# Performance work log

Measured on AMD Instinct MI355X. Metric: run time of the kernel, lower is better.

## Reference

```python
import jax, jax.numpy as jnp
import numpy as np

EMBED_DIM = 1024
HEADS = 16
D_HEAD = EMBED_DIM // HEADS
B, S = 4, 2048


def setup_inputs() -> dict:
    key = jax.random.key(0)
    ks = jax.random.split(key, 7)
    scale = 1.0 / np.sqrt(EMBED_DIM)
    inp = {
        "key": jax.random.normal(ks[0], (B, S, EMBED_DIM), jnp.float32),
        "query": jax.random.normal(ks[1], (B, S, EMBED_DIM), jnp.float32),
        "value": jax.random.normal(ks[2], (B, S, EMBED_DIM), jnp.float32),
        # causal boolean mask, broadcastable to [B, H, S, S]
        "mask": jnp.tril(jnp.ones((S, S), dtype=bool))[None, None, :, :] * jnp.ones((B, 1, 1, 1), dtype=bool),
        # nn.Linear weights, stored torch-style as [out_features, in_features]
        "Wq": jax.random.normal(ks[3], (EMBED_DIM, EMBED_DIM), jnp.float32) * scale,
        "Wk": jax.random.normal(ks[4], (EMBED_DIM, EMBED_DIM), jnp.float32) * scale,
        "Wv": jax.random.normal(ks[5], (EMBED_DIM, EMBED_DIM), jnp.float32) * scale,
        "Wo": jax.random.normal(ks[6], (EMBED_DIM, EMBED_DIM), jnp.float32) * scale,
    }
    return inp


def reference(key, query, value, mask, Wq, Wk, Wv, Wo):
    # projections (nn.Linear, bias=False): x @ W.T
    q = query @ Wq.T                                    # [B,S,E]
    k = key @ Wk.T
    v = value @ Wv.T
    # split heads -> [B,H,S,d]
    def split(x):
        return x.reshape(B, S, HEADS, D_HEAD).transpose(0, 2, 1, 3)
    q, k, v = split(q), split(k), split(v)
    # scaled dot-product scores [B,H,S,S]
    scores = jnp.einsum("bhqd,bhkd->bhqk", q, k) / np.sqrt(D_HEAD).astype(np.float32)
    scores = jnp.where(mask, scores, jnp.float32(-1e9))
    attn = jax.nn.softmax(scores, axis=-1)
    # attention output, merge heads
    out = jnp.einsum("bhqk,bhkd->bhqd", attn, v)        # [B,H,S,d]
    out = out.transpose(0, 2, 1, 3).reshape(B, S, EMBED_DIM)
    return out @ Wo.T
```

## Files before the change

### kernel.cpp

```cpp
#include <hip/hip_runtime.h>

#define SEQ 2048
#define EMBED 1024
#define DHEAD 64

typedef _Float16 h8 __attribute__((ext_vector_type(8)));
typedef _Float16 h4 __attribute__((ext_vector_type(4)));
typedef float f4 __attribute__((ext_vector_type(4)));
typedef unsigned int u32;

__device__ __forceinline__ void gload_lds16(const void* g, void* l) {
    __builtin_amdgcn_global_load_lds(
        (const __attribute__((address_space(1))) u32*)g,
        (__attribute__((address_space(3))) u32*)l, 16, 0, 0);
}

__global__ __launch_bounds__(256) void cvt_f16(
    const float* __restrict__ q, const float* __restrict__ k, const float* __restrict__ v,
    const float* __restrict__ wq, const float* __restrict__ wk, const float* __restrict__ wv,
    const float* __restrict__ wo,
    _Float16* __restrict__ q16, _Float16* __restrict__ k16, _Float16* __restrict__ v16,
    _Float16* __restrict__ wq16, _Float16* __restrict__ wk16, _Float16* __restrict__ wv16,
    _Float16* __restrict__ wo16)
{
    int bid = blockIdx.x;
    const float* src;
    _Float16* dst;
    float scale = 1.0f;
    size_t base;
    if (bid < 24576) {
        int seg = bid >> 13;
        base = (size_t)(bid & 8191) * 1024 + threadIdx.x * 4;
        src = seg == 0 ? q : seg == 1 ? k : v;
        dst = seg == 0 ? q16 : seg == 1 ? k16 : v16;
    } else {
        int wb = bid - 24576;
        int seg = wb >> 10;
        base = (size_t)(wb & 1023) * 1024 + threadIdx.x * 4;
        src = seg == 0 ? wq : seg == 1 ? wk : seg == 2 ? wv : wo;
        dst = seg == 0 ? wq16 : seg == 1 ? wk16 : seg == 2 ? wv16 : wo16;
        if (seg == 0) scale = 0.18033688011112042f;
    }
    float4 x = *(const float4*)(src + base);
    h4 y = { (_Float16)(x.x * scale), (_Float16)(x.y * scale),
             (_Float16)(x.z * scale), (_Float16)(x.w * scale) };
    *(h4*)(dst + base) = y;
}

__device__ __forceinline__ void gemm_core(const _Float16* __restrict__ A, const _Float16* __restrict__ W,
                                          int m0, int n0, int tid,
                                          _Float16* As, _Float16* Bs, f4 acc[4][4])
{
    const int lane = tid & 63, wave = tid >> 6;
    const int t16 = lane & 15, quad = lane >> 4;
    const int wm = (wave >> 1) * 64, wn = (wave & 1) * 64;
    const int rA = tid >> 2;
    const int cA = (tid & 3) * 8;
    const _Float16* ga = A + (size_t)(m0 + rA) * 1024 + cA;
    const _Float16* gb = W + (size_t)(n0 + rA) * 1024 + cA;
    _Float16* la = As + wave * 512;
    _Float16* lb = Bs + wave * 512;

    for (int k0 = 0; k0 < 1024; k0 += 64) {
        __syncthreads();
#pragma unroll
        for (int j = 0; j < 4; ++j) {
            const int roff = (j & 1) * 64;
            const int koff = (j >> 1) * 32;
            gload_lds16(ga + (size_t)roff * 1024 + k0 + koff, la + j * 2048);
            gload_lds16(gb + (size_t)roff * 1024 + k0 + koff, lb + j * 2048);
        }
        __syncthreads();
#pragma unroll
        for (int kk = 0; kk < 2; ++kk) {
            h8 af[4], bf[4];
#pragma unroll
            for (int i = 0; i < 4; ++i)
                af[i] = *(const h8*)(As + kk * 4096 + (wm + i * 16 + t16) * 32 + quad * 8);
#pragma unroll
            for (int j = 0; j < 4; ++j)
                bf[j] = *(const h8*)(Bs + kk * 4096 + (wn + j * 16 + t16) * 32 + quad * 8);
#pragma unroll
            for (int i = 0; i < 4; ++i)
#pragma unroll
                for (int j = 0; j < 4; ++j)
                    acc[i][j] = __builtin_amdgcn_mfma_f32_16x16x32_f16(af[i], bf[j], acc[i][j], 0, 0, 0);
        }
    }
}

__global__ __launch_bounds__(256) void proj_qkv(
    const _Float16* __restrict__ q16, const _Float16* __restrict__ k16, const _Float16* __restrict__ v16,
    const _Float16* __restrict__ Wq, const _Float16* __restrict__ Wk, const _Float16* __restrict__ Wv,
    _Float16* __restrict__ Qh, _Float16* __restrict__ Kh, _Float16* __restrict__ Vt)
{
    __shared__ _Float16 As[8192], Bs[8192];
    const int tid = threadIdx.x;
    const int z = blockIdx.z;
    const _Float16 *A, *W;
    int m0, n0;
    if (z == 2) { A = Wv; W = v16; m0 = blockIdx.y * 128; n0 = blockIdx.x * 128; }
    else if (z == 0) { A = q16; W = Wq; m0 = blockIdx.x * 128; n0 = blockIdx.y * 128; }
    else { A = k16; W = Wk; m0 = blockIdx.x * 128; n0 = blockIdx.y * 128; }

    f4 acc[4][4];
    const f4 z4 = {0.f, 0.f, 0.f, 0.f};
#pragma unroll
    for (int i = 0; i < 4; ++i)
#pragma unroll
        for (int j = 0; j < 4; ++j) acc[i][j] = z4;

    gemm_core(A, W, m0, n0, tid, As, Bs, acc);

    const int lane = tid & 63, wave = tid >> 6;
    const int t16 = lane & 15, quad = lane >> 4;
    const int wm = (wave >> 1) * 64, wn = (wave & 1) * 64;
#pragma unroll
    for (int i = 0; i < 4; ++i)
#pragma unroll
        for (int j = 0; j < 4; ++j)
#pragma unroll
            for (int reg = 0; reg < 4; ++reg) {
                int gm = m0 + wm + i * 16 + quad * 4 + reg;
                int gn = n0 + wn + j * 16 + t16;
                float vv = acc[i][j][reg];
                if (z < 2) {
                    int b = gm >> 11, s = gm & 2047, h = gn >> 6, dd = gn & 63;
                    _Float16* dst = (z == 0) ? Qh : Kh;
                    dst[(((size_t)(b * 16 + h) * SEQ) + s) * DHEAD + dd] = (_Float16)vv;
                } else {
                    int h = gm >> 6, dd = gm & 63, b = gn >> 11, s = gn & 2047;
                    int jt = s >> 6, ks = s & 63;
                    int j4 = ks >> 4, quadv = (ks >> 2) & 3, regv = ks & 3;
                    int dt = dd >> 4, t16v = dd & 15;
                    size_t off = (size_t)(b * 16 + h) * (SEQ * DHEAD)
                               + (size_t)(jt * 8 + dt * 2 + (j4 >> 1)) * 512
                               + (quadv * 16 + t16v) * 8 + (j4 & 1) * 4 + regv;
                    Vt[off] = (_Float16)vv;
                }
            }
}

__global__ __launch_bounds__(256) void attn3(
    const _Float16* __restrict__ Qh, const _Float16* __restrict__ Kh,
    const _Float16* __restrict__ Vt, _Float16* __restrict__ Ob)
{
    __shared__ _Float16 Kbuf[2][8][512];
    __shared__ _Float16 Vbuf[2][8][512];

    const int tid = threadIdx.x;
    const int lane = tid & 63, wave = tid >> 6;
    const int t16 = lane & 15, quad = lane >> 4;
    const int bh = blockIdx.x;
    const int b = bh >> 4, h = bh & 15;
    const int qb = (gridDim.y - 1) - blockIdx.y;
    const int q0 = qb * 128;
    const int nqt = qb * 2 + 2;

    const _Float16* Qp = Qh + (size_t)bh * SEQ * DHEAD;
    const _Float16* Kp = Kh + (size_t)bh * SEQ * DHEAD;
    const _Float16* Vp = Vt + (size_t)bh * SEQ * DHEAD;

    const int qlo[2] = { q0 + wave * 32, q0 + wave * 32 + 16 };
    const int last0 = (qlo[0] + 15) >> 6;

    h8 qf[2][2];
#pragma unroll
    for (int qb2 = 0; qb2 < 2; ++qb2)
#pragma unroll
        for (int kc = 0; kc < 2; ++kc)
            qf[qb2][kc] = *(const h8*)(Qp + (size_t)(qlo[qb2] + t16) * 64 + kc * 32 + quad * 8);

    const _Float16* Kl = Kp + t16 * 64 + quad * 8;
    const _Float16* Vl = Vp + lane * 8;

#define STAGE(jt_, bufi)                                                                  \
    do {                                                                                  \
        if (wave < 2) {                                                                   \
            _Pragma("unroll")                                                             \
            for (int i_ = 0; i_ < 4; ++i_) {                                              \
                int g_ = wave * 4 + i_;                                                   \
                gload_lds16(Kl + (jt_) * 4096 + (g_ >> 1) * 1024 + (g_ & 1) * 32,         \
                            &Kbuf[bufi][g_][0]);                                          \
            }                                                                             \
        } else {                                                                          \
            _Pragma("unroll")                                                             \
            for (int i_ = 0; i_ < 4; ++i_) {                                              \
                int g_ = (wave - 2) * 4 + i_;                                             \
                gload_lds16(Vl + ((jt_) * 8 + g_) * 512, &Vbuf[bufi][g_][0]);             \
            }                                                                             \
        }                                                                                 \
    } while (0)

    STAGE(0, 0);
    __syncthreads();

    float mv[2] = {-1e30f, -1e30f};
    float lv[2] = {0.f, 0.f};
    f4 o_acc[2][4];
    const f4 z4 = {0.f, 0.f, 0.f, 0.f};
#pragma unroll
    for (int qb2 = 0; qb2 < 2; ++qb2)
#pragma unroll
        for (int dt = 0; dt < 4; ++dt) o_acc[qb2][dt] = z4;

    for (int jt = 0; jt < nqt; ++jt) {
        const int buf = jt & 1;
        if (jt + 1 < nqt) STAGE(jt + 1, buf ^ 1);

        if (jt <= last0) {
            f4 s0[4], s1[4];
#pragma unroll
            for (int j4 = 0; j4 < 4; ++j4) {
                h8 kfa = *(const h8*)(&Kbuf[buf][j4 * 2 + 0][lane * 8]);
                h8 kfb = *(const h8*)(&Kbuf[buf][j4 * 2 + 1][lane * 8]);
                s1[j4] = __builtin_amdgcn_mfma_f32_16x16x32_f16(kfa, qf[1][0], z4, 0, 0, 0);
                s1[j4] = __builtin_amdgcn_mfma_f32_16x16x32_f16(kfb, qf[1][1], s1[j4], 0, 0, 0);
                s0[j4] = __builtin_amdgcn_mfma_f32_16x16x32_f16(kfa, qf[0][0], z4, 0, 0, 0);
                s0[j4] = __builtin_amdgcn_mfma_f32_16x16x32_f16(kfb, qf[0][1], s0[j4], 0, 0, 0);
            }

            h4 pf0[4], pf1[4];
            auto softmax_frag = [&](f4* s, int qb2, h4* pf) {
                const int myq = qlo[qb2] + t16;
                if ((jt << 6) + 63 > qlo[qb2]) {
#pragma unroll
                    for (int j4 = 0; j4 < 4; ++j4)
#pragma unroll
                        for (int reg = 0; reg < 4; ++reg) {
                            int kk = (jt << 6) + j4 * 16 + quad * 4 + reg;
                            if (kk > myq) s[j4][reg] = -1e30f;
                        }
                }
                float mr = s[0][0];
#pragma unroll
                for (int j4 = 0; j4 < 4; ++j4)
#pragma unroll
                    for (int reg = 0; reg < 4; ++reg) mr = fmaxf(mr, s[j4][reg]);
                mr = fmaxf(mr, __shfl_xor(mr, 16, 64));
                mr = fmaxf(mr, __shfl_xor(mr, 32, 64));
                float mn = mv[qb2];
                if (__any(mr > mn + 8.0f)) {
                    mn = fmaxf(mn, mr);
                    float al = __builtin_amdgcn_exp2f(mv[qb2] - mn);
                    mv[qb2] = mn;
                    lv[qb2] *= al;
#pragma unroll
                    for (int dt = 0; dt < 4; ++dt)
#pragma unroll
                        for (int reg = 0; reg < 4; ++reg) o_acc[qb2][dt][reg] *= al;
                }
                float rs = 0.f;
#pragma unroll
                for (int j4 = 0; j4 < 4; ++j4) {
#pragma unroll
                    for (int reg = 0; reg < 4; ++reg) {
                        float p = __builtin_amdgcn_exp2f(s[j4][reg] - mn);
                        s[j4][reg] = p;
                        rs += p;
                    }
                    pf[j4] = (h4){ (_Float16)s[j4][0], (_Float16)s[j4][1],
                                   (_Float16)s[j4][2], (_Float16)s[j4][3] };
                }
                rs += __shfl_xor(rs, 16, 64);
                rs += __shfl_xor(rs, 32, 64);
                lv[qb2] += rs;
            };
            softmax_frag(s0, 0, pf0);
            softmax_frag(s1, 1, pf1);

#pragma unroll
            for (int dt = 0; dt < 4; ++dt) {
#pragma unroll
                for (int j4p = 0; j4p < 2; ++j4p) {
                    h8 v2 = *(const h8*)(&Vbuf[buf][dt * 2 + j4p][lane * 8]);
                    h4 vlo = __builtin_shufflevector(v2, v2, 0, 1, 2, 3);
                    h4 vhi = __builtin_shufflevector(v2, v2, 4, 5, 6, 7);
                    o_acc[0][dt] = __builtin_amdgcn_mfma_f32_16x16x16f16(vlo, pf0[j4p * 2 + 0], o_acc[0][dt], 0, 0, 0);
                    o_acc[0][dt] = __builtin_amdgcn_mfma_f32_16x16x16f16(vhi, pf0[j4p * 2 + 1], o_acc[0][dt], 0, 0, 0);
                    o_acc[1][dt] = __builtin_amdgcn_mfma_f32_16x16x16f16(vlo, pf1[j4p * 2 + 0], o_acc[1][dt], 0, 0, 0);
                    o_acc[1][dt] = __builtin_amdgcn_mfma_f32_16x16x16f16(vhi, pf1[j4p * 2 + 1], o_acc[1][dt], 0, 0, 0);
                }
            }
        }
        __syncthreads();
    }

    _Float16* ep = ((_Float16*)Kbuf) + wave * 1024;
    const int swz = (t16 & 7) << 3;
#pragma unroll
    for (int qb2 = 0; qb2 < 2; ++qb2) {
        float inv = __builtin_amdgcn_rcpf(lv[qb2]);
#pragma unroll
        for (int dt = 0; dt < 4; ++dt) {
            h4 ov = { (_Float16)(o_acc[qb2][dt][0] * inv), (_Float16)(o_acc[qb2][dt][1] * inv),
                      (_Float16)(o_acc[qb2][dt][2] * inv), (_Float16)(o_acc[qb2][dt][3] * inv) };
            *(h4*)(ep + t16 * 64 + ((dt * 16 + quad * 4) ^ swz)) = ov;
        }
        h8 r0 = *(const h8*)(ep + t16 * 64 + ((quad * 8) ^ swz));
        h8 r1 = *(const h8*)(ep + t16 * 64 + ((32 + quad * 8) ^ swz));
        int s = qlo[qb2] + t16;
        _Float16* og = Ob + ((size_t)(b * SEQ + s)) * EMBED + h * DHEAD;
        *(h8*)(og + quad * 8) = r0;
        *(h8*)(og + 32 + quad * 8) = r1;
    }
#undef STAGE
}

__global__ __launch_bounds__(256) void proj_out(
    const _Float16* __restrict__ A, const _Float16* __restrict__ Wo, float* __restrict__ out)
{
    __shared__ _Float16 As[8192], Bs[8192];
    const int tid = threadIdx.x;
    const int m0 = blockIdx.x * 128, n0 = blockIdx.y * 128;
    f4 acc[4][4];
    const f4 z4 = {0.f, 0.f, 0.f, 0.f};
#pragma unroll
    for (int i = 0; i < 4; ++i)
#pragma unroll
        for (int j = 0; j < 4; ++j) acc[i][j] = z4;

    gemm_core(A, Wo, m0, n0, tid, As, Bs, acc);

    const int lane = tid & 63, wave = tid >> 6;
    const int t16 = lane & 15, quad = lane >> 4;
    const int wm = (wave >> 1) * 64, wn = (wave & 1) * 64;
#pragma unroll
    for (int i = 0; i < 4; ++i)
#pragma unroll
        for (int j = 0; j < 4; ++j)
#pragma unroll
            for (int reg = 0; reg < 4; ++reg) {
                int gm = m0 + wm + i * 16 + quad * 4 + reg;
                int gn = n0 + wn + j * 16 + t16;
                out[(size_t)gm * EMBED + gn] = acc[i][j][reg];
            }
}

extern "C" void kernel_launch(void* const* d_in, const int* in_sizes, int n_in,
                              void* d_out, int out_size, void* d_ws, size_t ws_size,
                              hipStream_t stream) {
    const float* key   = (const float*)d_in[0];
    const float* query = (const float*)d_in[1];
    const float* value = (const float*)d_in[2];
    const float* Wq = (const float*)d_in[4];
    const float* Wk = (const float*)d_in[5];
    const float* Wv = (const float*)d_in[6];
    const float* Wo = (const float*)d_in[7];

    char* ws = (char*)d_ws;
    _Float16* v16  = (_Float16*)(ws);
    _Float16* Wq16 = (_Float16*)(ws + (16u << 20));
    _Float16* Wk16 = (_Float16*)(ws + (18u << 20));
    _Float16* Wv16 = (_Float16*)(ws + (20u << 20));
    _Float16* Wo16 = (_Float16*)(ws + (22u << 20));
    _Float16* Qh   = (_Float16*)(ws + (24u << 20));
    _Float16* Kh   = (_Float16*)(ws + (40u << 20));
    _Float16* Vt   = (_Float16*)(ws + (56u << 20));
    _Float16* Ob   = v16;
    _Float16* q16 = (_Float16*)d_out;
    _Float16* k16 = (_Float16*)d_out + 8388608;

    dim3 blk(256);
    cvt_f16<<<dim3(28672), blk, 0, stream>>>(query, key, value, Wq, Wk, Wv, Wo,
                                             q16, k16, v16, Wq16, Wk16, Wv16, Wo16);
    proj_qkv<<<dim3(64, 8, 3), blk, 0, stream>>>(q16, k16, v16, Wq16, Wk16, Wv16, Qh, Kh, Vt);
    attn3<<<dim3(64, 16), blk, 0, stream>>>(Qh, Kh, Vt, Ob);
    proj_out<<<dim3(64, 8), blk, 0, stream>>>(Ob, Wo16, (float*)d_out);
}
```

Measured before the change: 351.3 us.

## Double-buffer LDS tiles in projection GEMM core with async prefetch

Restructures the GEMM main loop into a two-stage software pipeline. Each iteration issues the global-to-LDS loads for the next 32-wide K slice into the alternate buffer, then waits only on the current slice with a manual vmcnt wait and barrier before running the MFMAs. This overlaps memory latency with compute instead of loading and computing in lockstep. In exchange the K step per barrier halves, adding barriers, and the hand-written waitcnt counts must stay matched to the number of loads issued.

```diff
diff --git a/kernel.cpp b/kernel.cpp
--- a/kernel.cpp
+++ b/kernel.cpp
@@ -54,39 +54,52 @@
     const int lane = tid & 63, wave = tid >> 6;
     const int t16 = lane & 15, quad = lane >> 4;
     const int wm = (wave >> 1) * 64, wn = (wave & 1) * 64;
-    const int rA = tid >> 2;
-    const int cA = (tid & 3) * 8;
-    const _Float16* ga = A + (size_t)(m0 + rA) * 1024 + cA;
-    const _Float16* gb = W + (size_t)(n0 + rA) * 1024 + cA;
-    _Float16* la = As + wave * 512;
-    _Float16* lb = Bs + wave * 512;
-
-    for (int k0 = 0; k0 < 1024; k0 += 64) {
-        __syncthreads();
-#pragma unroll
-        for (int j = 0; j < 4; ++j) {
-            const int roff = (j & 1) * 64;
-            const int koff = (j >> 1) * 32;
-            gload_lds16(ga + (size_t)roff * 1024 + k0 + koff, la + j * 2048);
-            gload_lds16(gb + (size_t)roff * 1024 + k0 + koff, lb + j * 2048);
+    const int r0 = tid >> 2, c0 = (tid & 3) * 8;
+    const _Float16* ga0 = A + (size_t)(m0 + r0) * 1024 + c0;
+    const _Float16* ga1 = A + (size_t)(m0 + r0 + 64) * 1024 + c0;
+    const _Float16* gb0 = W + (size_t)(n0 + r0) * 1024 + c0;
+    const _Float16* gb1 = W + (size_t)(n0 + r0 + 64) * 1024 + c0;
+    _Float16* la0 = As + wave * 512;
+    _Float16* la1 = As + 2048 + wave * 512;
+    _Float16* lb0 = Bs + wave * 512;
+    _Float16* lb1 = Bs + 2048 + wave * 512;
+
+#define GSTAGE(k0_, b_)  do {                                  \
+        gload_lds16(ga0 + (k0_), la0 + (b_) * 4096);           \
+        gload_lds16(ga1 + (k0_), la1 + (b_) * 4096);           \
+        gload_lds16(gb0 + (k0_), lb0 + (b_) * 4096);           \
+        gload_lds16(gb1 + (k0_), lb1 + (b_) * 4096);           \
+    } while (0)
+
+    GSTAGE(0, 0);
+#pragma unroll 2
+    for (int k = 0; k < 32; ++k) {
+        const int b = k & 1;
+        if (k < 31) {
+            GSTAGE((k + 1) * 32, b ^ 1);
+            asm volatile("s_waitcnt vmcnt(4)\n\ts_barrier" ::: "memory");
+        } else {
+            asm volatile("s_waitcnt vmcnt(0)\n\ts_barrier" ::: "memory");
         }
-        __syncthreads();
-#pragma unroll
-        for (int kk = 0; kk < 2; ++kk) {
-            h8 af[4], bf[4];
-#pragma unroll
-            for (int i = 0; i < 4; ++i)
-                af[i] = *(const h8*)(As + kk * 4096 + (wm + i * 16 + t16) * 32 + quad * 8);
+        __builtin_amdgcn_sched_barrier(0);
+        const _Float16* As_ = As + b * 4096;
+        const _Float16* Bs_ = Bs + b * 4096;
+        h8 af[4], bf[4];
+#pragma unroll
+        for (int i = 0; i < 4; ++i)
+            af[i] = *(const h8*)(As_ + (wm + i * 16 + t16) * 32 + quad * 8);
+#pragma unroll
+        for (int j = 0; j < 4; ++j)
+            bf[j] = *(const h8*)(Bs_ + (wn + j * 16 + t16) * 32 + quad * 8);
+#pragma unroll
+        for (int i = 0; i < 4; ++i)
 #pragma unroll
             for (int j = 0; j < 4; ++j)
-                bf[j] = *(const h8*)(Bs + kk * 4096 + (wn + j * 16 + t16) * 32 + quad * 8);
-#pragma unroll
-            for (int i = 0; i < 4; ++i)
-#pragma unroll
-                for (int j = 0; j < 4; ++j)
-                    acc[i][j] = __builtin_amdgcn_mfma_f32_16x16x32_f16(af[i], bf[j], acc[i][j], 0, 0, 0);
-        }
+                acc[i][j] = __builtin_amdgcn_mfma_f32_16x16x32_f16(af[i], bf[j], acc[i][j], 0, 0, 0);
+        __builtin_amdgcn_sched_barrier(0);
+        asm volatile("s_barrier" ::: "memory");
     }
+#undef GSTAGE
 }
 
 __global__ __launch_bounds__(256) void proj_qkv(
```

Result: no change. 351.1 us (-0.0%).
